# Performance work log

Measured on AMD Instinct MI355X. Metric: run time of the kernel, lower is better.

Reference implementation:

```python
import jax, jax.numpy as jnp
import numpy as np

T, N, E = 8, 10000, 200000
F_IN, H, OUT = 32, 128, 64
EPS = 1e-5


def setup_inputs() -> dict:
    key = jax.random.key(0)
    ks = jax.random.split(key, 28)
    inp = {}
    inp['x'] = jax.random.normal(ks[0], (T, N, F_IN), jnp.float32)
    inp['edge_index'] = jax.random.randint(ks[1], (2, E), 0, N, dtype=jnp.int32)
    # GCN layer weights (Glorot-ish scale)
    inp['w_gcn0'] = jax.random.normal(ks[2], (F_IN, H), jnp.float32) / np.float32(np.sqrt(F_IN))
    inp['b_gcn0'] = jnp.zeros((H,), jnp.float32)
    inp['w_gcn1'] = jax.random.normal(ks[3], (H, H), jnp.float32) / np.float32(np.sqrt(H))
    inp['b_gcn1'] = jnp.zeros((H,), jnp.float32)
    inp['w_gcn2'] = jax.random.normal(ks[4], (H, H), jnp.float32) / np.float32(np.sqrt(H))
    inp['b_gcn2'] = jnp.zeros((H,), jnp.float32)
    # BatchNorm (eval mode) params for the two inner norms
    for i, kb in zip(range(2), range(5, 9, 2)):
        inp[f'bn_g{i}'] = 1.0 + 0.1 * jax.random.normal(ks[kb], (H,), jnp.float32)
        inp[f'bn_b{i}'] = 0.1 * jax.random.normal(ks[kb + 1], (H,), jnp.float32)
        inp[f'bn_m{i}'] = 0.1 * jax.random.normal(ks[kb + 10], (H,), jnp.float32)
        inp[f'bn_v{i}'] = jax.random.uniform(ks[kb + 11], (H,), jnp.float32, 0.5, 1.5)
    # 3-layer LSTM params, torch gate order (i, f, g, o)
    s = np.float32(1.0 / np.sqrt(OUT))
    dims_in = [H, OUT, OUT]
    for l in range(3):
        k0, k1, k2, k3 = jax.random.split(ks[20 + l], 4)
        inp[f'w_ih_{l}'] = jax.random.uniform(k0, (4 * OUT, dims_in[l]), jnp.float32, -s, s)
        inp[f'w_hh_{l}'] = jax.random.uniform(k1, (4 * OUT, OUT), jnp.float32, -s, s)
        inp[f'b_ih_{l}'] = jax.random.uniform(k2, (4 * OUT,), jnp.float32, -s, s)
        inp[f'b_hh_{l}'] = jax.random.uniform(k3, (4 * OUT,), jnp.float32, -s, s)
    return inp


def reference(x, edge_index, w_gcn0, b_gcn0, w_gcn1, b_gcn1, w_gcn2, b_gcn2,
              bn_g0, bn_b0, bn_m0, bn_v0, bn_g1, bn_b1, bn_m1, bn_v1,
              w_ih_0, w_hh_0, b_ih_0, b_hh_0,
              w_ih_1, w_hh_1, b_ih_1, b_hh_1,
              w_ih_2, w_hh_2, b_ih_2, b_hh_2):
    src, dst = edge_index[0], edge_index[1]
    # symmetric GCN normalization with self-loops: deg = in-degree + 1
    deg = jax.ops.segment_sum(jnp.ones((E,), x.dtype), dst, num_segments=N) + 1.0
    dis = jax.lax.rsqrt(deg)
    coef = dis[src] * dis[dst]          # [E] edge norm
    self_w = dis * dis                   # [N] self-loop norm

    def gcn(h, W, b):
        hw = jnp.einsum('tnf,fo->tno', h, W)                      # [T,N,O]
        msg = hw[:, src, :] * coef[None, :, None]                  # [T,E,O]
        agg = jax.vmap(lambda m: jax.ops.segment_sum(m, dst, num_segments=N))(msg)
        return agg + hw * self_w[None, :, None] + b

    def bn(h, g, b_, m, v):  # eval-mode BatchNorm1d
        return (h - m) * (g * jax.lax.rsqrt(v + EPS)) + b_

    h = bn(jax.nn.relu(gcn(x, w_gcn0, b_gcn0)), bn_g0, bn_b0, bn_m0, bn_v0)
    h = bn(jax.nn.relu(gcn(h, w_gcn1, b_gcn1)), bn_g1, bn_b1, bn_m1, bn_v1)
    h = jax.nn.relu(gcn(h, w_gcn2, b_gcn2))                        # [T,N,H]

    def lstm_layer(xs, Wih, Whh, bih, bhh):
        Hd = Whh.shape[1]
        bias = bih + bhh
        def step(carry, xt):
            hp, cp = carry
            g = xt @ Wih.T + hp @ Whh.T + bias
            i, f, gg, o = jnp.split(g, 4, axis=-1)
            c = jax.nn.sigmoid(f) * cp + jax.nn.sigmoid(i) * jnp.tanh(gg)
            hn = jax.nn.sigmoid(o) * jnp.tanh(c)
            return (hn, c), hn
        z = jnp.zeros((xs.shape[1], Hd), xs.dtype)
        _, ys = jax.lax.scan(step, (z, z), xs)
        return ys  # [T,N,Hd]

    ys = lstm_layer(h, w_ih_0, w_hh_0, b_ih_0, b_hh_0)
    ys = lstm_layer(ys, w_ih_1, w_hh_1, b_ih_1, b_hh_1)
    ys = lstm_layer(ys, w_ih_2, w_hh_2, b_ih_2, b_hh_2)
    return ys[-1]  # [N, OUT] == x[:, -1, :] in the torch code
```

## Files before the change

### kernel.cpp

```cpp
#include <hip/hip_runtime.h>
#include <hip/hip_bf16.h>
#include <math.h>

#define NTHREADS 256
#define T_STEPS 8
#define F_INC 32
#define H_DIM 128
#define O_DIM 64

typedef unsigned short u16;
typedef __attribute__((ext_vector_type(8))) short short8_t;
typedef __attribute__((ext_vector_type(4))) float float4_t;
typedef __attribute__((ext_vector_type(2))) float float2_t;

__device__ __forceinline__ float bf2f(u16 u) {
    return __uint_as_float(((unsigned)u) << 16);
}
__device__ __forceinline__ u16 f2bf(float f) {
    __hip_bfloat16 h = __float2bfloat16(f);
    union { __hip_bfloat16 h; u16 s; } cv; cv.h = h; return cv.s;
}
__device__ __forceinline__ float2_t bfpair(unsigned u) {
    union { unsigned w[2]; float2_t f; } c;
    c.w[0] = u << 16;
    c.w[1] = u & 0xffff0000u;
    return c.f;
}
__device__ __forceinline__ void bf8_unpack(uint4 u, float* f) {
    f[0] = __uint_as_float(u.x << 16); f[1] = __uint_as_float(u.x & 0xffff0000u);
    f[2] = __uint_as_float(u.y << 16); f[3] = __uint_as_float(u.y & 0xffff0000u);
    f[4] = __uint_as_float(u.z << 16); f[5] = __uint_as_float(u.z & 0xffff0000u);
    f[6] = __uint_as_float(u.w << 16); f[7] = __uint_as_float(u.w & 0xffff0000u);
}
__device__ __forceinline__ float fsig(float x) {
    float xc = fminf(fmaxf(x, -30.f), 30.f);
    float e = __builtin_amdgcn_exp2f(xc * -1.4426950408889634f);
    return __builtin_amdgcn_rcpf(1.0f + e);
}
__device__ __forceinline__ float ftanh(float x) {
    float xc = fminf(fmaxf(x, -15.f), 15.f);
    float e = __builtin_amdgcn_exp2f(xc * -2.8853900817779268f);
    float r = __builtin_amdgcn_rcpf(1.0f + e);
    return fmaf(-2.0f * e, r, 1.0f);
}

__global__ void count_kernel(const int* __restrict__ ei, int* __restrict__ cnt, int E) {
    int e = blockIdx.x * NTHREADS + threadIdx.x;
    if (e < E) atomicAdd(&cnt[ei[E + e]], 1);
}

__global__ void scan_part1(const int* __restrict__ cnt, int* __restrict__ bsum, int n) {
    __shared__ int sd[NTHREADS];
    const int i = blockIdx.x * NTHREADS + threadIdx.x;
    sd[threadIdx.x] = (i < n) ? cnt[i] : 0;
    __syncthreads();
    for (int off = 128; off > 0; off >>= 1) {
        if (threadIdx.x < off) sd[threadIdx.x] += sd[threadIdx.x + off];
        __syncthreads();
    }
    if (threadIdx.x == 0) bsum[blockIdx.x] = sd[0];
}

__global__ void scan_part3(const int* __restrict__ cnt, const int* __restrict__ bsum,
                           int* __restrict__ rowptr, int* __restrict__ wp,
                           float* __restrict__ dis, float* __restrict__ selfw, int n) {
    __shared__ int sd[NTHREADS];
    __shared__ int sbase;
    const int tid = threadIdx.x;
    if (tid < 64) {
        int v0 = (tid < blockIdx.x) ? bsum[tid] : 0;
        #pragma unroll
        for (int off = 1; off < 64; off <<= 1) v0 += __shfl_xor(v0, off);
        if (tid == 0) sbase = v0;
    }
    const int i = blockIdx.x * NTHREADS + tid;
    const int v = (i < n) ? cnt[i] : 0;
    sd[tid] = v;
    __syncthreads();
    for (int off = 1; off < NTHREADS; off <<= 1) {
        const int tv = (tid >= off) ? sd[tid - off] : 0;
        __syncthreads();
        sd[tid] += tv;
        __syncthreads();
    }
    const int excl = sbase + sd[tid] - v;
    if (i < n) {
        rowptr[i] = excl; wp[i] = excl;
        if (i == n - 1) rowptr[n] = excl + v;
        const float d = 1.0f + (float)v;
        dis[i] = rsqrtf(d);
        selfw[i] = 1.0f / d;
    }
}

__global__ void fill_kernel(const int* __restrict__ ei, const float* __restrict__ dis,
                            int* __restrict__ wp, int2* __restrict__ epk, int E) {
    int e = blockIdx.x * NTHREADS + threadIdx.x;
    if (e < E) {
        int s = ei[e], d = ei[E + e];
        int p = atomicAdd(&wp[d], 1);
        epk[p] = make_int2(s, __float_as_int(dis[s] * dis[d]));
    }
}

__global__ void wprep_all_kernel(const float* g0, const float* g1, const float* g2,
                                 const float* i0, const float* i1, const float* i2,
                                 const float* h0, const float* h1, const float* h2,
                                 u16* o_g0, u16* o_g1, u16* o_g2,
                                 u16* o_i0, u16* o_i1, u16* o_i2,
                                 u16* o_h0, u16* o_h1, u16* o_h2) {
    const int i = blockIdx.x * NTHREADS + threadIdx.x;
    if (i < 4096)        { o_g0[i] = f2bf(g0[(i & 31) * 128 + (i >> 5)]); }
    else if (i < 20480)  { int j = i - 4096;   o_g1[j] = f2bf(g1[(j & 127) * 128 + (j >> 7)]); }
    else if (i < 36864)  { int j = i - 20480;  o_g2[j] = f2bf(g2[(j & 127) * 128 + (j >> 7)]); }
    else if (i < 69632)  { int j = i - 36864;  o_i0[j] = f2bf(i0[j]); }
    else if (i < 86016)  { int j = i - 69632;  o_i1[j] = f2bf(i1[j]); }
    else if (i < 102400) { int j = i - 86016;  o_i2[j] = f2bf(i2[j]); }
    else if (i < 118784) { int j = i - 102400; o_h0[j] = f2bf(h0[j]); }
    else if (i < 135168) { int j = i - 118784; o_h1[j] = f2bf(h1[j]); }
    else if (i < 151552) { int j = i - 135168; o_h2[j] = f2bf(h2[j]); }
}

__global__ __launch_bounds__(NTHREADS)
void gcn32_kernel(const float* __restrict__ x, const int* __restrict__ rowptr,
                  const int2* __restrict__ epk,
                  const float* __restrict__ selfw, const u16* __restrict__ Wt,
                  const float* __restrict__ bias,
                  const float* __restrict__ bng, const float* __restrict__ bnb,
                  const float* __restrict__ bnm, const float* __restrict__ bnv,
                  u16* __restrict__ out, int N) {
    constexpr int ASTR = 40;
    constexpr int ECAP = 1024;
    __shared__ __align__(16) u16 aT[2][16][ASTR];
    __shared__ int2 sM[ECAP];
    const int t0 = blockIdx.x * 2;
    const int n0 = blockIdx.y * 16;
    const int tid = threadIdx.x;
    const int wid = tid >> 6, lane = tid & 63;
    const int quad = lane >> 4, l16 = lane & 15;
    const float* xb0 = x + (long)t0 * N * 32;
    const float* xb1 = xb0 + (long)N * 32;

    const int eb0 = rowptr[n0];
    const int ecnt = min(rowptr[n0 + 16] - eb0, ECAP);
    for (int p = tid; p < ecnt; p += NTHREADS) sM[p] = epk[eb0 + p];
    __syncthreads();

    const int split = lane >> 3;
    const int c4 = (lane & 7) * 4;
    for (int i = 0; i < 4; ++i) {
        const int n = n0 + wid * 4 + i;
        const int l0 = rowptr[n] - eb0;
        const int l1 = rowptr[n + 1] - eb0;
        const int eL = min(l1, ecnt);
        const int start = l0 + split;
        float2_t a0[2] = {(float2_t){0.f, 0.f}, (float2_t){0.f, 0.f}};
        float2_t a1[2] = {(float2_t){0.f, 0.f}, (float2_t){0.f, 0.f}};
        #pragma unroll 2
        for (int e = start; e < eL; e += 8) {
            const int2 m = sM[e];
            const float w = __int_as_float(m.y);
            const float2_t w2 = {w, w};
            const long o = (long)m.x * 32 + c4;
            const float4 v0 = *(const float4*)(xb0 + o);
            const float4 v1 = *(const float4*)(xb1 + o);
            a0[0] = __builtin_elementwise_fma((float2_t){v0.x, v0.y}, w2, a0[0]);
            a0[1] = __builtin_elementwise_fma((float2_t){v0.z, v0.w}, w2, a0[1]);
            a1[0] = __builtin_elementwise_fma((float2_t){v1.x, v1.y}, w2, a1[0]);
            a1[1] = __builtin_elementwise_fma((float2_t){v1.z, v1.w}, w2, a1[1]);
        }
        const int kL = (eL > start) ? (eL - start + 7) >> 3 : 0;
        for (int e = start + kL * 8; e < l1; e += 8) {
            const int2 m = epk[eb0 + e];
            const float w = __int_as_float(m.y);
            const float2_t w2 = {w, w};
            const long o = (long)m.x * 32 + c4;
            const float4 v0 = *(const float4*)(xb0 + o);
            const float4 v1 = *(const float4*)(xb1 + o);
            a0[0] = __builtin_elementwise_fma((float2_t){v0.x, v0.y}, w2, a0[0]);
            a0[1] = __builtin_elementwise_fma((float2_t){v0.z, v0.w}, w2, a0[1]);
            a1[0] = __builtin_elementwise_fma((float2_t){v1.x, v1.y}, w2, a1[0]);
            a1[1] = __builtin_elementwise_fma((float2_t){v1.z, v1.w}, w2, a1[1]);
        }
        float r[8] = {a0[0][0], a0[0][1], a0[1][0], a0[1][1],
                      a1[0][0], a1[0][1], a1[1][0], a1[1][1]};
        #pragma unroll
        for (int j = 0; j < 8; ++j) {
            r[j] += __shfl_xor(r[j], 8);
            r[j] += __shfl_xor(r[j], 16);
            r[j] += __shfl_xor(r[j], 32);
        }
        if (split == 0) {
            const float sw = selfw[n];
            const float4 s0 = *(const float4*)(xb0 + (long)n * 32 + c4);
            const float4 s1 = *(const float4*)(xb1 + (long)n * 32 + c4);
            ushort4 o0, o1;
            o0.x = f2bf(fmaf(sw, s0.x, r[0])); o0.y = f2bf(fmaf(sw, s0.y, r[1]));
            o0.z = f2bf(fmaf(sw, s0.z, r[2])); o0.w = f2bf(fmaf(sw, s0.w, r[3]));
            o1.x = f2bf(fmaf(sw, s1.x, r[4])); o1.y = f2bf(fmaf(sw, s1.y, r[5]));
            o1.z = f2bf(fmaf(sw, s1.z, r[6])); o1.w = f2bf(fmaf(sw, s1.w, r[7]));
            *(ushort4*)(&aT[0][wid * 4 + i][c4]) = o0;
            *(ushort4*)(&aT[1][wid * 4 + i][c4]) = o1;
        }
    }
    __syncthreads();

    const short8_t fA0 = *(const short8_t*)(&aT[0][l16][quad * 8]);
    const short8_t fA1 = *(const short8_t*)(&aT[1][l16][quad * 8]);
    float4_t acc[2][2];
    short8_t fB[2];
    #pragma unroll
    for (int ct = 0; ct < 2; ++ct) {
        const int col = wid * 32 + ct * 16 + l16;
        fB[ct] = *(const short8_t*)(Wt + (long)col * 32 + quad * 8);
        acc[0][ct] = (float4_t){0.f, 0.f, 0.f, 0.f};
        acc[1][ct] = (float4_t){0.f, 0.f, 0.f, 0.f};
    }
    #pragma unroll
    for (int ct = 0; ct < 2; ++ct) {
        acc[0][ct] = __builtin_amdgcn_mfma_f32_16x16x32_bf16(fA0, fB[ct], acc[0][ct], 0, 0, 0);
        acc[1][ct] = __builtin_amdgcn_mfma_f32_16x16x32_bf16(fA1, fB[ct], acc[1][ct], 0, 0, 0);
    }

    #pragma unroll
    for (int ct = 0; ct < 2; ++ct) {
        const int c = wid * 32 + ct * 16 + l16;
        const float s = bng[c] * rsqrtf(bnv[c] + 1e-5f);
        const float a1 = bnb[c] - bnm[c] * s;
        const float a0 = bias[c];
        #pragma unroll
        for (int tt = 0; tt < 2; ++tt) {
            #pragma unroll
            for (int r = 0; r < 4; ++r) {
                const int node = quad * 4 + r;
                float v = fmaf(fmaxf(acc[tt][ct][r] + a0, 0.f), s, a1);
                out[((long)(t0 + tt) * N + n0 + node) * 128 + c] = f2bf(v);
            }
        }
    }
}

template<int EPI>
__global__ __launch_bounds__(NTHREADS)
void gcn128_kernel(const u16* __restrict__ h, const int* __restrict__ rowptr,
                   const int2* __restrict__ epk,
                   const float* __restrict__ selfw, const u16* __restrict__ Wt,
                   const float* __restrict__ bias,
                   const float* __restrict__ bng, const float* __restrict__ bnb,
                   const float* __restrict__ bnm, const float* __restrict__ bnv,
                   u16* __restrict__ out, int N) {
    constexpr int ASTR = 136;
    constexpr int ECAP = 1024;
    __shared__ __align__(16) u16 aT[16][ASTR];
    __shared__ int2 sM[ECAP];
    const int t = blockIdx.x;
    const int n0 = blockIdx.y * 16;
    const int tid = threadIdx.x;
    const int wid = tid >> 6, lane = tid & 63;
    const int quad = lane >> 4, l16 = lane & 15;
    const u16* hb = h + (long)t * N * 128;

    const int eb0 = rowptr[n0];
    const int ecnt = min(rowptr[n0 + 16] - eb0, ECAP);
    for (int p = tid; p < ecnt; p += NTHREADS) sM[p] = epk[eb0 + p];
    __syncthreads();

    const int split = lane >> 4;
    const int c8 = l16 * 8;
    for (int i = 0; i < 4; ++i) {
        const int n = n0 + wid * 4 + i;
        const int l0 = rowptr[n] - eb0;
        const int l1 = rowptr[n + 1] - eb0;
        const int eL = min(l1, ecnt);
        const int start = l0 + split;
        float2_t a2[4] = {(float2_t){0.f, 0.f}, (float2_t){0.f, 0.f},
                          (float2_t){0.f, 0.f}, (float2_t){0.f, 0.f}};
        #pragma unroll 4
        for (int e = start; e < eL; e += 4) {
            const int2 m = sM[e];
            const float w = __int_as_float(m.y);
            const float2_t w2 = {w, w};
            const uint4 v = *(const uint4*)(hb + (long)m.x * 128 + c8);
            a2[0] = __builtin_elementwise_fma(bfpair(v.x), w2, a2[0]);
            a2[1] = __builtin_elementwise_fma(bfpair(v.y), w2, a2[1]);
            a2[2] = __builtin_elementwise_fma(bfpair(v.z), w2, a2[2]);
            a2[3] = __builtin_elementwise_fma(bfpair(v.w), w2, a2[3]);
        }
        const int kL = (eL > start) ? (eL - start + 3) >> 2 : 0;
        for (int e = start + kL * 4; e < l1; e += 4) {
            const int2 m = epk[eb0 + e];
            const float w = __int_as_float(m.y);
            const float2_t w2 = {w, w};
            const uint4 v = *(const uint4*)(hb + (long)m.x * 128 + c8);
            a2[0] = __builtin_elementwise_fma(bfpair(v.x), w2, a2[0]);
            a2[1] = __builtin_elementwise_fma(bfpair(v.y), w2, a2[1]);
            a2[2] = __builtin_elementwise_fma(bfpair(v.z), w2, a2[2]);
            a2[3] = __builtin_elementwise_fma(bfpair(v.w), w2, a2[3]);
        }
        float a[8] = {a2[0][0], a2[0][1], a2[1][0], a2[1][1],
                      a2[2][0], a2[2][1], a2[3][0], a2[3][1]};
        #pragma unroll
        for (int j = 0; j < 8; ++j) {
            a[j] += __shfl_xor(a[j], 16);
            a[j] += __shfl_xor(a[j], 32);
        }
        if (split == 0) {
            const float sw = selfw[n];
            const uint4 sv = *(const uint4*)(hb + (long)n * 128 + c8);
            float f[8];
            bf8_unpack(sv, f);
            ushort4 o0, o1;
            o0.x = f2bf(fmaf(sw, f[0], a[0])); o0.y = f2bf(fmaf(sw, f[1], a[1]));
            o0.z = f2bf(fmaf(sw, f[2], a[2])); o0.w = f2bf(fmaf(sw, f[3], a[3]));
            o1.x = f2bf(fmaf(sw, f[4], a[4])); o1.y = f2bf(fmaf(sw, f[5], a[5]));
            o1.z = f2bf(fmaf(sw, f[6], a[6])); o1.w = f2bf(fmaf(sw, f[7], a[7]));
            *(ushort4*)(&aT[wid * 4 + i][c8]) = o0;
            *(ushort4*)(&aT[wid * 4 + i][c8 + 4]) = o1;
        }
    }
    __syncthreads();

    short8_t fA[4];
    #pragma unroll
    for (int ks = 0; ks < 4; ++ks)
        fA[ks] = *(const short8_t*)(&aT[l16][ks * 32 + quad * 8]);
    float4_t acc[2];
    #pragma unroll
    for (int ct = 0; ct < 2; ++ct) acc[ct] = (float4_t){0.f, 0.f, 0.f, 0.f};
    #pragma unroll
    for (int ct = 0; ct < 2; ++ct) {
        const int col = wid * 32 + ct * 16 + l16;
        #pragma unroll
        for (int ks = 0; ks < 4; ++ks) {
            const short8_t fB = *(const short8_t*)(Wt + (long)col * 128 + ks * 32 + quad * 8);
            acc[ct] = __builtin_amdgcn_mfma_f32_16x16x32_bf16(fA[ks], fB, acc[ct], 0, 0, 0);
        }
    }

    #pragma unroll
    for (int ct = 0; ct < 2; ++ct) {
        const int c = wid * 32 + ct * 16 + l16;
        const float a0 = bias[c];
        float s = 0.f, a1 = 0.f;
        if constexpr (EPI == 2) {
            s = bng[c] * rsqrtf(bnv[c] + 1e-5f);
            a1 = bnb[c] - bnm[c] * s;
        }
        #pragma unroll
        for (int r = 0; r < 4; ++r) {
            const int node = quad * 4 + r;
            float v = fmaxf(acc[ct][r] + a0, 0.f);
            if constexpr (EPI == 2) v = fmaf(v, s, a1);
            out[((long)t * N + n0 + node) * 128 + c] = f2bf(v);
        }
    }
}

template<int KIN, bool IN_SPLIT, bool LAST>
__global__ __launch_bounds__(NTHREADS, 2)
void lstm_layer_kernel(const u16* __restrict__ in_hi, const u16* __restrict__ in_lo,
                       const u16* __restrict__ wih, const u16* __restrict__ whh,
                       const float* __restrict__ bi, const float* __restrict__ bh,
                       u16* __restrict__ out_hi, u16* __restrict__ out_lo,
                       float* __restrict__ out_f, int N) {
    constexpr int NKS = KIN / 32;
    constexpr int HSTR = 76;
    const int tid = threadIdx.x;
    const int w = tid >> 6, lane = tid & 63;
    const int quad = lane >> 4, l16 = lane & 15;
    const int n0 = blockIdx.x * 16;
    const int u = w * 16 + l16;

    __shared__ __align__(16) u16 hT[2][16][HSTR];
    for (int p = tid; p < 2 * 16 * HSTR; p += NTHREADS) (&hT[0][0][0])[p] = 0;

    short8_t fI[4][NKS], fH[4][2];
    #pragma unroll
    for (int g = 0; g < 4; ++g) {
        #pragma unroll
        for (int ks = 0; ks < NKS; ++ks)
            fI[g][ks] = *(const short8_t*)(wih + (long)(g * 64 + u) * KIN + ks * 32 + quad * 8);
        #pragma unroll
        for (int ks = 0; ks < 2; ++ks)
            fH[g][ks] = *(const short8_t*)(whh + (long)(g * 64 + u) * 64 + ks * 32 + quad * 8);
    }
    float bias[4];
    #pragma unroll
    for (int g = 0; g < 4; ++g) bias[g] = bi[g * 64 + u] + bh[g * 64 + u];
    float cst[4] = {};
    __syncthreads();

    #pragma unroll 1
    for (int t = 0; t < T_STEPS; ++t) {
        short8_t ain[NKS], ainl[NKS];
        const long ibase = ((long)t * N + n0 + l16) * KIN + quad * 8;
        #pragma unroll
        for (int ks = 0; ks < NKS; ++ks) {
            ain[ks] = *(const short8_t*)(in_hi + ibase + ks * 32);
            if constexpr (IN_SPLIT) ainl[ks] = *(const short8_t*)(in_lo + ibase + ks * 32);
        }
        short8_t ah[2], al[2];
        #pragma unroll
        for (int ks = 0; ks < 2; ++ks) {
            ah[ks] = *(const short8_t*)(&hT[0][l16][ks * 32 + quad * 8]);
            al[ks] = *(const short8_t*)(&hT[1][l16][ks * 32 + quad * 8]);
        }
        __syncthreads();

        float4_t acc[4];
        #pragma unroll
        for (int g = 0; g < 4; ++g) acc[g] = (float4_t){bias[g], bias[g], bias[g], bias[g]};
        #pragma unroll
        for (int ks = 0; ks < NKS; ++ks)
            #pragma unroll
            for (int g = 0; g < 4; ++g) {
                acc[g] = __builtin_amdgcn_mfma_f32_16x16x32_bf16(ain[ks], fI[g][ks], acc[g], 0, 0, 0);
                if constexpr (IN_SPLIT)
                    acc[g] = __builtin_amdgcn_mfma_f32_16x16x32_bf16(ainl[ks], fI[g][ks], acc[g], 0, 0, 0);
            }
        #pragma unroll
        for (int ks = 0; ks < 2; ++ks)
            #pragma unroll
            for (int g = 0; g < 4; ++g) {
                acc[g] = __builtin_amdgcn_mfma_f32_16x16x32_bf16(ah[ks], fH[g][ks], acc[g], 0, 0, 0);
                acc[g] = __builtin_amdgcn_mfma_f32_16x16x32_bf16(al[ks], fH[g][ks], acc[g], 0, 0, 0);
            }

        #pragma unroll
        for (int r = 0; r < 4; ++r) {
            const float si = fsig(acc[0][r]);
            const float sf = fsig(acc[1][r]);
            const float gg = ftanh(acc[2][r]);
            const float so = fsig(acc[3][r]);
            const float c = sf * cst[r] + si * gg;
            cst[r] = c;
            const float h = so * ftanh(c);
            const int node = quad * 4 + r;
            const u16 hi = f2bf(h);
            const u16 lo = f2bf(h - bf2f(hi));
            hT[0][node][u] = hi;
            hT[1][node][u] = lo;
            if constexpr (LAST) {
                if (t == T_STEPS - 1) out_f[(long)(n0 + node) * 64 + u] = h;
            } else {
                const long o = ((long)t * N + n0 + node) * 64 + u;
                out_hi[o] = hi;
                out_lo[o] = lo;
            }
        }
        __syncthreads();
    }
}

extern "C" void kernel_launch(void* const* d_in, const int* in_sizes, int n_in,
                              void* d_out, int out_size, void* d_ws, size_t ws_size,
                              hipStream_t stream) {
    (void)n_in; (void)out_size; (void)ws_size;
    const float* x      = (const float*)d_in[0];
    const int*   ei     = (const int*)d_in[1];
    const float* w_gcn0 = (const float*)d_in[2];
    const float* b_gcn0 = (const float*)d_in[3];
    const float* w_gcn1 = (const float*)d_in[4];
    const float* b_gcn1 = (const float*)d_in[5];
    const float* w_gcn2 = (const float*)d_in[6];
    const float* b_gcn2 = (const float*)d_in[7];
    const float* bn_g0  = (const float*)d_in[8];
    const float* bn_b0  = (const float*)d_in[9];
    const float* bn_m0  = (const float*)d_in[10];
    const float* bn_v0  = (const float*)d_in[11];
    const float* bn_g1  = (const float*)d_in[12];
    const float* bn_b1  = (const float*)d_in[13];
    const float* bn_m1  = (const float*)d_in[14];
    const float* bn_v1  = (const float*)d_in[15];
    const float* w_ih_0 = (const float*)d_in[16];
    const float* w_hh_0 = (const float*)d_in[17];
    const float* b_ih_0 = (const float*)d_in[18];
    const float* b_hh_0 = (const float*)d_in[19];
    const float* w_ih_1 = (const float*)d_in[20];
    const float* w_hh_1 = (const float*)d_in[21];
    const float* b_ih_1 = (const float*)d_in[22];
    const float* b_hh_1 = (const float*)d_in[23];
    const float* w_ih_2 = (const float*)d_in[24];
    const float* w_hh_2 = (const float*)d_in[25];
    const float* b_ih_2 = (const float*)d_in[26];
    const float* b_hh_2 = (const float*)d_in[27];

    const int E = in_sizes[1] / 2;
    const int N = in_sizes[0] / (T_STEPS * F_INC);
    const long M = (long)N * T_STEPS;

    char* ws = (char*)d_ws;
    size_t off = 0;
    auto carve = [&](size_t bytes) -> void* {
        void* p = ws + off;
        off += (bytes + 255) & ~(size_t)255;
        return p;
    };
    float* dis     = (float*)carve((size_t)N * 4);
    float* selfw   = (float*)carve((size_t)N * 4);
    int*   cnt     = (int*)carve((size_t)N * 4);
    int*   rowptr  = (int*)carve((size_t)(N + 1) * 4);
    int*   wp      = (int*)carve((size_t)N * 4);
    int2*  epk     = (int2*)carve((size_t)E * 8);
    int*   bsum    = (int*)carve(64 * 4);
    u16*   hbuf    = (u16*)carve((size_t)M * H_DIM * 2);
    u16*   hbuf2   = (u16*)carve((size_t)M * H_DIM * 2);
    u16*   pA_hi   = (u16*)carve((size_t)M * O_DIM * 2);
    u16*   pA_lo   = (u16*)carve((size_t)M * O_DIM * 2);
    u16*   pB_hi   = (u16*)carve((size_t)M * O_DIM * 2);
    u16*   pB_lo   = (u16*)carve((size_t)M * O_DIM * 2);
    u16*   wt0     = (u16*)carve((size_t)128 * 32 * 2);
    u16*   wt1     = (u16*)carve((size_t)128 * 128 * 2);
    u16*   wt2     = (u16*)carve((size_t)128 * 128 * 2);
    u16*   wtih0   = (u16*)carve((size_t)256 * 128 * 2);
    u16*   wtih1   = (u16*)carve((size_t)256 * 64 * 2);
    u16*   wtih2   = (u16*)carve((size_t)256 * 64 * 2);
    u16*   whh0b   = (u16*)carve((size_t)256 * 64 * 2);
    u16*   whh1b   = (u16*)carve((size_t)256 * 64 * 2);
    u16*   whh2b   = (u16*)carve((size_t)256 * 64 * 2);

    const dim3 b256(NTHREADS);
    const int gN = (N + NTHREADS - 1) / NTHREADS;
    const int gE = (E + NTHREADS - 1) / NTHREADS;

    hipMemsetAsync(cnt, 0, (size_t)N * 4, stream);
    count_kernel<<<gE, b256, 0, stream>>>(ei, cnt, E);
    scan_part1<<<gN, b256, 0, stream>>>(cnt, bsum, N);
    scan_part3<<<gN, b256, 0, stream>>>(cnt, bsum, rowptr, wp, dis, selfw, N);
    fill_kernel<<<gE, b256, 0, stream>>>(ei, dis, wp, epk, E);

    wprep_all_kernel<<<(151552 + 255) / 256, b256, 0, stream>>>(
        w_gcn0, w_gcn1, w_gcn2, w_ih_0, w_ih_1, w_ih_2, w_hh_0, w_hh_1, w_hh_2,
        wt0, wt1, wt2, wtih0, wtih1, wtih2, whh0b, whh1b, whh2b);

    gcn32_kernel<<<dim3(T_STEPS / 2, N / 16), b256, 0, stream>>>(
        x, rowptr, epk, selfw, wt0, b_gcn0,
        bn_g0, bn_b0, bn_m0, bn_v0, hbuf, N);
    const dim3 gG(T_STEPS, N / 16);
    gcn128_kernel<2><<<gG, b256, 0, stream>>>(
        hbuf, rowptr, epk, selfw, wt1, b_gcn1,
        bn_g1, bn_b1, bn_m1, bn_v1, hbuf2, N);
    gcn128_kernel<1><<<gG, b256, 0, stream>>>(
        hbuf2, rowptr, epk, selfw, wt2, b_gcn2,
        nullptr, nullptr, nullptr, nullptr, hbuf, N);

    const int gL = N / 16;
    lstm_layer_kernel<128, false, false><<<gL, b256, 0, stream>>>(
        hbuf, nullptr, wtih0, whh0b, b_ih_0, b_hh_0, pA_hi, pA_lo, nullptr, N);
    lstm_layer_kernel<64, true, false><<<gL, b256, 0, stream>>>(
        pA_hi, pA_lo, wtih1, whh1b, b_ih_1, b_hh_1, pB_hi, pB_lo, nullptr, N);
    lstm_layer_kernel<64, true, true><<<gL, b256, 0, stream>>>(
        pB_hi, pB_lo, wtih2, whh2b, b_ih_2, b_hh_2, nullptr, nullptr, (float*)d_out, N);
}
```

Before: 356.6 us.

## Fuse LSTM layers 1-2, process two timesteps per GCN128 block, merge prep kernels

Runs LSTM layers 1 and 2 together in a single kernel, passing layer-1 hidden state to layer 2 through shared memory. This removes the intermediate hi/lo global buffers and one launch. The GCN128 kernel now handles two timesteps per block, so the CSR edge list is staged once and the weight fragments are reused across both timesteps. The degree-count kernel is merged with the weight-prep kernel to save another launch. In exchange, the fused kernels use more registers and shared memory, and the GCN128 grid has half as many blocks.

```diff
diff --git a/kernel.cpp b/kernel.cpp
--- a/kernel.cpp
+++ b/kernel.cpp
@@ -44,72 +44,20 @@
     return fmaf(-2.0f * e, r, 1.0f);
 }
 
-__global__ void count_kernel(const int* __restrict__ ei, int* __restrict__ cnt, int E) {
-    int e = blockIdx.x * NTHREADS + threadIdx.x;
-    if (e < E) atomicAdd(&cnt[ei[E + e]], 1);
-}
-
-__global__ void scan_part1(const int* __restrict__ cnt, int* __restrict__ bsum, int n) {
-    __shared__ int sd[NTHREADS];
-    const int i = blockIdx.x * NTHREADS + threadIdx.x;
-    sd[threadIdx.x] = (i < n) ? cnt[i] : 0;
-    __syncthreads();
-    for (int off = 128; off > 0; off >>= 1) {
-        if (threadIdx.x < off) sd[threadIdx.x] += sd[threadIdx.x + off];
-        __syncthreads();
-    }
-    if (threadIdx.x == 0) bsum[blockIdx.x] = sd[0];
-}
-
-__global__ void scan_part3(const int* __restrict__ cnt, const int* __restrict__ bsum,
-                           int* __restrict__ rowptr, int* __restrict__ wp,
-                           float* __restrict__ dis, float* __restrict__ selfw, int n) {
-    __shared__ int sd[NTHREADS];
-    __shared__ int sbase;
-    const int tid = threadIdx.x;
-    if (tid < 64) {
-        int v0 = (tid < blockIdx.x) ? bsum[tid] : 0;
-        #pragma unroll
-        for (int off = 1; off < 64; off <<= 1) v0 += __shfl_xor(v0, off);
-        if (tid == 0) sbase = v0;
-    }
-    const int i = blockIdx.x * NTHREADS + tid;
-    const int v = (i < n) ? cnt[i] : 0;
-    sd[tid] = v;
-    __syncthreads();
-    for (int off = 1; off < NTHREADS; off <<= 1) {
-        const int tv = (tid >= off) ? sd[tid - off] : 0;
-        __syncthreads();
-        sd[tid] += tv;
-        __syncthreads();
-    }
-    const int excl = sbase + sd[tid] - v;
-    if (i < n) {
-        rowptr[i] = excl; wp[i] = excl;
-        if (i == n - 1) rowptr[n] = excl + v;
-        const float d = 1.0f + (float)v;
-        dis[i] = rsqrtf(d);
-        selfw[i] = 1.0f / d;
-    }
-}
-
-__global__ void fill_kernel(const int* __restrict__ ei, const float* __restrict__ dis,
-                            int* __restrict__ wp, int2* __restrict__ epk, int E) {
-    int e = blockIdx.x * NTHREADS + threadIdx.x;
-    if (e < E) {
-        int s = ei[e], d = ei[E + e];
-        int p = atomicAdd(&wp[d], 1);
-        epk[p] = make_int2(s, __float_as_int(dis[s] * dis[d]));
-    }
-}
-
-__global__ void wprep_all_kernel(const float* g0, const float* g1, const float* g2,
-                                 const float* i0, const float* i1, const float* i2,
-                                 const float* h0, const float* h1, const float* h2,
-                                 u16* o_g0, u16* o_g1, u16* o_g2,
-                                 u16* o_i0, u16* o_i1, u16* o_i2,
-                                 u16* o_h0, u16* o_h1, u16* o_h2) {
-    const int i = blockIdx.x * NTHREADS + threadIdx.x;
+__global__ void count_wprep_kernel(const int* __restrict__ ei, int* __restrict__ cnt,
+                                   int E, int gE,
+                                   const float* g0, const float* g1, const float* g2,
+                                   const float* i0, const float* i1, const float* i2,
+                                   const float* h0, const float* h1, const float* h2,
+                                   u16* o_g0, u16* o_g1, u16* o_g2,
+                                   u16* o_i0, u16* o_i1, u16* o_i2,
+                                   u16* o_h0, u16* o_h1, u16* o_h2) {
+    if ((int)blockIdx.x < gE) {
+        int e = blockIdx.x * NTHREADS + threadIdx.x;
+        if (e < E) atomicAdd(&cnt[ei[E + e]], 1);
+        return;
+    }
+    const int i = (blockIdx.x - gE) * NTHREADS + threadIdx.x;
     if (i < 4096)        { o_g0[i] = f2bf(g0[(i & 31) * 128 + (i >> 5)]); }
     else if (i < 20480)  { int j = i - 4096;   o_g1[j] = f2bf(g1[(j & 127) * 128 + (j >> 7)]); }
     else if (i < 36864)  { int j = i - 20480;  o_g2[j] = f2bf(g2[(j & 127) * 128 + (j >> 7)]); }
@@ -119,6 +67,60 @@
     else if (i < 118784) { int j = i - 102400; o_h0[j] = f2bf(h0[j]); }
     else if (i < 135168) { int j = i - 118784; o_h1[j] = f2bf(h1[j]); }
     else if (i < 151552) { int j = i - 135168; o_h2[j] = f2bf(h2[j]); }
+}
+
+__global__ void scan_part1(const int* __restrict__ cnt, int* __restrict__ bsum, int n) {
+    __shared__ int sd[NTHREADS];
+    const int i = blockIdx.x * NTHREADS + threadIdx.x;
+    sd[threadIdx.x] = (i < n) ? cnt[i] : 0;
+    __syncthreads();
+    for (int off = 128; off > 0; off >>= 1) {
+        if (threadIdx.x < off) sd[threadIdx.x] += sd[threadIdx.x + off];
+        __syncthreads();
+    }
+    if (threadIdx.x == 0) bsum[blockIdx.x] = sd[0];
+}
+
+__global__ void scan_part3(const int* __restrict__ cnt, const int* __restrict__ bsum,
+                           int* __restrict__ rowptr, int* __restrict__ wp,
+                           float* __restrict__ dis, float* __restrict__ selfw, int n) {
+    __shared__ int sd[NTHREADS];
+    __shared__ int sbase;
+    const int tid = threadIdx.x;
+    if (tid < 64) {
+        int v0 = (tid < blockIdx.x) ? bsum[tid] : 0;
+        #pragma unroll
+        for (int off = 1; off < 64; off <<= 1) v0 += __shfl_xor(v0, off);
+        if (tid == 0) sbase = v0;
+    }
+    const int i = blockIdx.x * NTHREADS + tid;
+    const int v = (i < n) ? cnt[i] : 0;
+    sd[tid] = v;
+    __syncthreads();
+    for (int off = 1; off < NTHREADS; off <<= 1) {
+        const int tv = (tid >= off) ? sd[tid - off] : 0;
+        __syncthreads();
+        sd[tid] += tv;
+        __syncthreads();
+    }
+    const int excl = sbase + sd[tid] - v;
+    if (i < n) {
+        rowptr[i] = excl; wp[i] = excl;
+        if (i == n - 1) rowptr[n] = excl + v;
+        const float d = 1.0f + (float)v;
+        dis[i] = rsqrtf(d);
+        selfw[i] = 1.0f / d;
+    }
+}
+
+__global__ void fill_kernel(const int* __restrict__ ei, const float* __restrict__ dis,
+                            int* __restrict__ wp, int2* __restrict__ epk, int E) {
+    int e = blockIdx.x * NTHREADS + threadIdx.x;
+    if (e < E) {
+        int s = ei[e], d = ei[E + e];
+        int p = atomicAdd(&wp[d], 1);
+        epk[p] = make_int2(s, __float_as_int(dis[s] * dis[d]));
+    }
 }
 
 __global__ __launch_bounds__(NTHREADS)
@@ -251,14 +253,15 @@
                    u16* __restrict__ out, int N) {
     constexpr int ASTR = 136;
     constexpr int ECAP = 1024;
-    __shared__ __align__(16) u16 aT[16][ASTR];
+    __shared__ __align__(16) u16 aT[2][16][ASTR];
     __shared__ int2 sM[ECAP];
-    const int t = blockIdx.x;
+    const int t0 = blockIdx.x * 2;
     const int n0 = blockIdx.y * 16;
     const int tid = threadIdx.x;
     const int wid = tid >> 6, lane = tid & 63;
     const int quad = lane >> 4, l16 = lane & 15;
-    const u16* hb = h + (long)t * N * 128;
+    const u16* hb0 = h + (long)t0 * N * 128;
+    const u16* hb1 = hb0 + (long)N * 128;
 
     const int eb0 = rowptr[n0];
     const int ecnt = min(rowptr[n0 + 16] - eb0, ECAP);
@@ -273,67 +276,96 @@
         const int l1 = rowptr[n + 1] - eb0;
         const int eL = min(l1, ecnt);
         const int start = l0 + split;
-        float2_t a2[4] = {(float2_t){0.f, 0.f}, (float2_t){0.f, 0.f},
+        float2_t aA[4] = {(float2_t){0.f, 0.f}, (float2_t){0.f, 0.f},
+                          (float2_t){0.f, 0.f}, (float2_t){0.f, 0.f}};
+        float2_t aB[4] = {(float2_t){0.f, 0.f}, (float2_t){0.f, 0.f},
                           (float2_t){0.f, 0.f}, (float2_t){0.f, 0.f}};
         #pragma unroll 4
         for (int e = start; e < eL; e += 4) {
             const int2 m = sM[e];
             const float w = __int_as_float(m.y);
             const float2_t w2 = {w, w};
-            const uint4 v = *(const uint4*)(hb + (long)m.x * 128 + c8);
-            a2[0] = __builtin_elementwise_fma(bfpair(v.x), w2, a2[0]);
-            a2[1] = __builtin_elementwise_fma(bfpair(v.y), w2, a2[1]);
-            a2[2] = __builtin_elementwise_fma(bfpair(v.z), w2, a2[2]);
-            a2[3] = __builtin_elementwise_fma(bfpair(v.w), w2, a2[3]);
+            const long o = (long)m.x * 128 + c8;
+            const uint4 v0 = *(const uint4*)(hb0 + o);
+            const uint4 v1 = *(const uint4*)(hb1 + o);
+            aA[0] = __builtin_elementwise_fma(bfpair(v0.x), w2, aA[0]);
+            aA[1] = __builtin_elementwise_fma(bfpair(v0.y), w2, aA[1]);
+            aA[2] = __builtin_elementwise_fma(bfpair(v0.z), w2, aA[2]);
+            aA[3] = __builtin_elementwise_fma(bfpair(v0.w), w2, aA[3]);
+            aB[0] = __builtin_elementwise_fma(bfpair(v1.x), w2, aB[0]);
+            aB[1] = __builtin_elementwise_fma(bfpair(v1.y), w2, aB[1]);
+            aB[2] = __builtin_elementwise_fma(bfpair(v1.z), w2, aB[2]);
+            aB[3] = __builtin_elementwise_fma(bfpair(v1.w), w2, aB[3]);
         }
         const int kL = (eL > start) ? (eL - start + 3) >> 2 : 0;
         for (int e = start + kL * 4; e < l1; e += 4) {
             const int2 m = epk[eb0 + e];
             const float w = __int_as_float(m.y);
             const float2_t w2 = {w, w};
-            const uint4 v = *(const uint4*)(hb + (long)m.x * 128 + c8);
-            a2[0] = __builtin_elementwise_fma(bfpair(v.x), w2, a2[0]);
-            a2[1] = __builtin_elementwise_fma(bfpair(v.y), w2, a2[1]);
-            a2[2] = __builtin_elementwise_fma(bfpair(v.z), w2, a2[2]);
-            a2[3] = __builtin_elementwise_fma(bfpair(v.w), w2, a2[3]);
-        }
-        float a[8] = {a2[0][0], a2[0][1], a2[1][0], a2[1][1],
-                      a2[2][0], a2[2][1], a2[3][0], a2[3][1]};
-        #pragma unroll
-        for (int j = 0; j < 8; ++j) {
+            const long o = (long)m.x * 128 + c8;
+            const uint4 v0 = *(const uint4*)(hb0 + o);
+            const uint4 v1 = *(const uint4*)(hb1 + o);
+            aA[0] = __builtin_elementwise_fma(bfpair(v0.x), w2, aA[0]);
+            aA[1] = __builtin_elementwise_fma(bfpair(v0.y), w2, aA[1]);
+            aA[2] = __builtin_elementwise_fma(bfpair(v0.z), w2, aA[2]);
+            aA[3] = __builtin_elementwise_fma(bfpair(v0.w), w2, aA[3]);
+            aB[0] = __builtin_elementwise_fma(bfpair(v1.x), w2, aB[0]);
+            aB[1] = __builtin_elementwise_fma(bfpair(v1.y), w2, aB[1]);
+            aB[2] = __builtin_elementwise_fma(bfpair(v1.z), w2, aB[2]);
+            aB[3] = __builtin_elementwise_fma(bfpair(v1.w), w2, aB[3]);
+        }
+        float a[16] = {aA[0][0], aA[0][1], aA[1][0], aA[1][1],
+                       aA[2][0], aA[2][1], aA[3][0], aA[3][1],
+                       aB[0][0], aB[0][1], aB[1][0], aB[1][1],
+                       aB[2][0], aB[2][1], aB[3][0], aB[3][1]};
+        #pragma unroll
+        for (int j = 0; j < 16; ++j) {
             a[j] += __shfl_xor(a[j], 16);
             a[j] += __shfl_xor(a[j], 32);
         }
         if (split == 0) {
             const float sw = selfw[n];
-            const uint4 sv = *(const uint4*)(hb + (long)n * 128 + c8);
-            float f[8];
-            bf8_unpack(sv, f);
-            ushort4 o0, o1;
-            o0.x = f2bf(fmaf(sw, f[0], a[0])); o0.y = f2bf(fmaf(sw, f[1], a[1]));
-            o0.z = f2bf(fmaf(sw, f[2], a[2])); o0.w = f2bf(fmaf(sw, f[3], a[3]));
-            o1.x = f2bf(fmaf(sw, f[4], a[4])); o1.y = f2bf(fmaf(sw, f[5], a[5]));
-            o1.z = f2bf(fmaf(sw, f[6], a[6])); o1.w = f2bf(fmaf(sw, f[7], a[7]));
-            *(ushort4*)(&aT[wid * 4 + i][c8]) = o0;
-            *(ushort4*)(&aT[wid * 4 + i][c8 + 4]) = o1;
-        }
-    }
-    __syncthreads();
-
-    short8_t fA[4];
-    #pragma unroll
-    for (int ks = 0; ks < 4; ++ks)
-        fA[ks] = *(const short8_t*)(&aT[l16][ks * 32 + quad * 8]);
-    float4_t acc[2];
-    #pragma unroll
-    for (int ct = 0; ct < 2; ++ct) acc[ct] = (float4_t){0.f, 0.f, 0.f, 0.f};
+            const uint4 s0 = *(const uint4*)(hb0 + (long)n * 128 + c8);
+            const uint4 s1 = *(const uint4*)(hb1 + (long)n * 128 + c8);
+            float f0[8], f1[8];
+            bf8_unpack(s0, f0);
+            bf8_unpack(s1, f1);
+            ushort4 oA0, oA1, oB0, oB1;
+            oA0.x = f2bf(fmaf(sw, f0[0], a[0]));  oA0.y = f2bf(fmaf(sw, f0[1], a[1]));
+            oA0.z = f2bf(fmaf(sw, f0[2], a[2]));  oA0.w = f2bf(fmaf(sw, f0[3], a[3]));
+            oA1.x = f2bf(fmaf(sw, f0[4], a[4]));  oA1.y = f2bf(fmaf(sw, f0[5], a[5]));
+            oA1.z = f2bf(fmaf(sw, f0[6], a[6]));  oA1.w = f2bf(fmaf(sw, f0[7], a[7]));
+            oB0.x = f2bf(fmaf(sw, f1[0], a[8]));  oB0.y = f2bf(fmaf(sw, f1[1], a[9]));
+            oB0.z = f2bf(fmaf(sw, f1[2], a[10])); oB0.w = f2bf(fmaf(sw, f1[3], a[11]));
+            oB1.x = f2bf(fmaf(sw, f1[4], a[12])); oB1.y = f2bf(fmaf(sw, f1[5], a[13]));
+            oB1.z = f2bf(fmaf(sw, f1[6], a[14])); oB1.w = f2bf(fmaf(sw, f1[7], a[15]));
+            *(ushort4*)(&aT[0][wid * 4 + i][c8]) = oA0;
+            *(ushort4*)(&aT[0][wid * 4 + i][c8 + 4]) = oA1;
+            *(ushort4*)(&aT[1][wid * 4 + i][c8]) = oB0;
+            *(ushort4*)(&aT[1][wid * 4 + i][c8 + 4]) = oB1;
+        }
+    }
+    __syncthreads();
+
+    short8_t fA0[4], fA1[4];
+    #pragma unroll
+    for (int ks = 0; ks < 4; ++ks) {
+        fA0[ks] = *(const short8_t*)(&aT[0][l16][ks * 32 + quad * 8]);
+        fA1[ks] = *(const short8_t*)(&aT[1][l16][ks * 32 + quad * 8]);
+    }
+    float4_t acc[2][2];
+    #pragma unroll
+    for (int tt = 0; tt < 2; ++tt)
+        #pragma unroll
+        for (int ct = 0; ct < 2; ++ct) acc[tt][ct] = (float4_t){0.f, 0.f, 0.f, 0.f};
     #pragma unroll
     for (int ct = 0; ct < 2; ++ct) {
         const int col = wid * 32 + ct * 16 + l16;
         #pragma unroll
         for (int ks = 0; ks < 4; ++ks) {
             const short8_t fB = *(const short8_t*)(Wt + (long)col * 128 + ks * 32 + quad * 8);
-            acc[ct] = __builtin_amdgcn_mfma_f32_16x16x32_bf16(fA[ks], fB, acc[ct], 0, 0, 0);
+            acc[0][ct] = __builtin_amdgcn_mfma_f32_16x16x32_bf16(fA0[ks], fB, acc[0][ct], 0, 0, 0);
+            acc[1][ct] = __builtin_amdgcn_mfma_f32_16x16x32_bf16(fA1[ks], fB, acc[1][ct], 0, 0, 0);
         }
     }
 
@@ -347,23 +379,23 @@
             a1 = bnb[c] - bnm[c] * s;
         }
         #pragma unroll
-        for (int r = 0; r < 4; ++r) {
-            const int node = quad * 4 + r;
-            float v = fmaxf(acc[ct][r] + a0, 0.f);
-            if constexpr (EPI == 2) v = fmaf(v, s, a1);
-            out[((long)t * N + n0 + node) * 128 + c] = f2bf(v);
-        }
-    }
-}
-
-template<int KIN, bool IN_SPLIT, bool LAST>
+        for (int tt = 0; tt < 2; ++tt) {
+            #pragma unroll
+            for (int r = 0; r < 4; ++r) {
+                const int node = quad * 4 + r;
+                float v = fmaxf(acc[tt][ct][r] + a0, 0.f);
+                if constexpr (EPI == 2) v = fmaf(v, s, a1);
+                out[((long)(t0 + tt) * N + n0 + node) * 128 + c] = f2bf(v);
+            }
+        }
+    }
+}
+
 __global__ __launch_bounds__(NTHREADS, 2)
-void lstm_layer_kernel(const u16* __restrict__ in_hi, const u16* __restrict__ in_lo,
-                       const u16* __restrict__ wih, const u16* __restrict__ whh,
-                       const float* __restrict__ bi, const float* __restrict__ bh,
-                       u16* __restrict__ out_hi, u16* __restrict__ out_lo,
-                       float* __restrict__ out_f, int N) {
-    constexpr int NKS = KIN / 32;
+void lstm0_kernel(const u16* __restrict__ in_h, const u16* __restrict__ wih,
+                  const u16* __restrict__ whh,
+                  const float* __restrict__ bi, const float* __restrict__ bh,
+                  u16* __restrict__ out_hi, u16* __restrict__ out_lo, int N) {
     constexpr int HSTR = 76;
     const int tid = threadIdx.x;
     const int w = tid >> 6, lane = tid & 63;
@@ -374,12 +406,12 @@
     __shared__ __align__(16) u16 hT[2][16][HSTR];
     for (int p = tid; p < 2 * 16 * HSTR; p += NTHREADS) (&hT[0][0][0])[p] = 0;
 
-    short8_t fI[4][NKS], fH[4][2];
+    short8_t fI[4][4], fH[4][2];
     #pragma unroll
     for (int g = 0; g < 4; ++g) {
         #pragma unroll
-        for (int ks = 0; ks < NKS; ++ks)
-            fI[g][ks] = *(const short8_t*)(wih + (long)(g * 64 + u) * KIN + ks * 32 + quad * 8);
+        for (int ks = 0; ks < 4; ++ks)
+            fI[g][ks] = *(const short8_t*)(wih + (long)(g * 64 + u) * 128 + ks * 32 + quad * 8);
         #pragma unroll
         for (int ks = 0; ks < 2; ++ks)
             fH[g][ks] = *(const short8_t*)(whh + (long)(g * 64 + u) * 64 + ks * 32 + quad * 8);
@@ -392,13 +424,11 @@
 
     #pragma unroll 1
     for (int t = 0; t < T_STEPS; ++t) {
-        short8_t ain[NKS], ainl[NKS];
-        const long ibase = ((long)t * N + n0 + l16) * KIN + quad * 8;
-        #pragma unroll
-        for (int ks = 0; ks < NKS; ++ks) {
-            ain[ks] = *(const short8_t*)(in_hi + ibase + ks * 32);
-            if constexpr (IN_SPLIT) ainl[ks] = *(const short8_t*)(in_lo + ibase + ks * 32);
-        }
+        short8_t ain[4];
+        const long ibase = ((long)t * N + n0 + l16) * 128 + quad * 8;
+        #pragma unroll
+        for (int ks = 0; ks < 4; ++ks)
+            ain[ks] = *(const short8_t*)(in_h + ibase + ks * 32);
         short8_t ah[2], al[2];
         #pragma unroll
         for (int ks = 0; ks < 2; ++ks) {
@@ -411,13 +441,10 @@
         #pragma unroll
         for (int g = 0; g < 4; ++g) acc[g] = (float4_t){bias[g], bias[g], bias[g], bias[g]};
         #pragma unroll
-        for (int ks = 0; ks < NKS; ++ks)
+        for (int ks = 0; ks < 4; ++ks)
             #pragma unroll
-            for (int g = 0; g < 4; ++g) {
+            for (int g = 0; g < 4; ++g)
                 acc[g] = __builtin_amdgcn_mfma_f32_16x16x32_bf16(ain[ks], fI[g][ks], acc[g], 0, 0, 0);
-                if constexpr (IN_SPLIT)
-                    acc[g] = __builtin_amdgcn_mfma_f32_16x16x32_bf16(ainl[ks], fI[g][ks], acc[g], 0, 0, 0);
-            }
         #pragma unroll
         for (int ks = 0; ks < 2; ++ks)
             #pragma unroll
@@ -440,12 +467,126 @@
             const u16 lo = f2bf(h - bf2f(hi));
             hT[0][node][u] = hi;
             hT[1][node][u] = lo;
-            if constexpr (LAST) {
-                if (t == T_STEPS - 1) out_f[(long)(n0 + node) * 64 + u] = h;
+            const long o = ((long)t * N + n0 + node) * 64 + u;
+            out_hi[o] = hi;
+            out_lo[o] = lo;
+        }
+        __syncthreads();
+    }
+}
+
+__global__ __launch_bounds__(NTHREADS)
+void lstm12_kernel(const u16* __restrict__ in_hi, const u16* __restrict__ in_lo,
+                   const u16* __restrict__ wih1, const u16* __restrict__ whh1,
+                   const u16* __restrict__ wih2, const u16* __restrict__ whh2,
+                   const float* __restrict__ bi1, const float* __restrict__ bh1,
+                   const float* __restrict__ bi2, const float* __restrict__ bh2,
+                   float* __restrict__ out_f, int N) {
+    constexpr int HSTR = 76;
+    const int tid = threadIdx.x;
+    const int w = tid >> 6, lane = tid & 63;
+    const int quad = lane >> 4, l16 = lane & 15;
+    const int n0 = blockIdx.x * 16;
+    const int u = w * 16 + l16;
+
+    __shared__ __align__(16) u16 hT[2][2][16][HSTR];
+    for (int p = tid; p < 2 * 2 * 16 * HSTR; p += NTHREADS) (&hT[0][0][0][0])[p] = 0;
+
+    short8_t fI1[4][2], fH1[4][2], fI2[4][2], fH2[4][2];
+    #pragma unroll
+    for (int g = 0; g < 4; ++g)
+        #pragma unroll
+        for (int ks = 0; ks < 2; ++ks) {
+            fI1[g][ks] = *(const short8_t*)(wih1 + (long)(g * 64 + u) * 64 + ks * 32 + quad * 8);
+            fH1[g][ks] = *(const short8_t*)(whh1 + (long)(g * 64 + u) * 64 + ks * 32 + quad * 8);
+            fI2[g][ks] = *(const short8_t*)(wih2 + (long)(g * 64 + u) * 64 + ks * 32 + quad * 8);
+            fH2[g][ks] = *(const short8_t*)(whh2 + (long)(g * 64 + u) * 64 + ks * 32 + quad * 8);
+        }
+    float b1[4], b2[4];
+    #pragma unroll
+    for (int g = 0; g < 4; ++g) {
+        b1[g] = bi1[g * 64 + u] + bh1[g * 64 + u];
+        b2[g] = bi2[g * 64 + u] + bh2[g * 64 + u];
+    }
+    float c1[4] = {}, c2[4] = {};
+    __syncthreads();
+
+    #pragma unroll 1
+    for (int t = 0; t < T_STEPS; ++t) {
+        short8_t ainh[2], ainl[2], r1h[2], r1l[2], r2h[2], r2l[2];
+        const long ibase = ((long)t * N + n0 + l16) * 64 + quad * 8;
+        #pragma unroll
+        for (int ks = 0; ks < 2; ++ks) {
+            ainh[ks] = *(const short8_t*)(in_hi + ibase + ks * 32);
+            ainl[ks] = *(const short8_t*)(in_lo + ibase + ks * 32);
+            r1h[ks] = *(const short8_t*)(&hT[0][0][l16][ks * 32 + quad * 8]);
+            r1l[ks] = *(const short8_t*)(&hT[0][1][l16][ks * 32 + quad * 8]);
+            r2h[ks] = *(const short8_t*)(&hT[1][0][l16][ks * 32 + quad * 8]);
+            r2l[ks] = *(const short8_t*)(&hT[1][1][l16][ks * 32 + quad * 8]);
+        }
+        __syncthreads();
+
+        float4_t acc[4];
+        #pragma unroll
+        for (int g = 0; g < 4; ++g) acc[g] = (float4_t){b1[g], b1[g], b1[g], b1[g]};
+        #pragma unroll
+        for (int ks = 0; ks < 2; ++ks)
+            #pragma unroll
+            for (int g = 0; g < 4; ++g) {
+                acc[g] = __builtin_amdgcn_mfma_f32_16x16x32_bf16(ainh[ks], fI1[g][ks], acc[g], 0, 0, 0);
+                acc[g] = __builtin_amdgcn_mfma_f32_16x16x32_bf16(ainl[ks], fI1[g][ks], acc[g], 0, 0, 0);
+                acc[g] = __builtin_amdgcn_mfma_f32_16x16x32_bf16(r1h[ks], fH1[g][ks], acc[g], 0, 0, 0);
+                acc[g] = __builtin_amdgcn_mfma_f32_16x16x32_bf16(r1l[ks], fH1[g][ks], acc[g], 0, 0, 0);
+            }
+        #pragma unroll
+        for (int r = 0; r < 4; ++r) {
+            const float si = fsig(acc[0][r]);
+            const float sf = fsig(acc[1][r]);
+            const float gg = ftanh(acc[2][r]);
+            const float so = fsig(acc[3][r]);
+            const float c = sf * c1[r] + si * gg;
+            c1[r] = c;
+            const float h = so * ftanh(c);
+            const int node = quad * 4 + r;
+            const u16 hi = f2bf(h);
+            hT[0][0][node][u] = hi;
+            hT[0][1][node][u] = f2bf(h - bf2f(hi));
+        }
+        __syncthreads();
+
+        short8_t i2h[2], i2l[2];
+        #pragma unroll
+        for (int ks = 0; ks < 2; ++ks) {
+            i2h[ks] = *(const short8_t*)(&hT[0][0][l16][ks * 32 + quad * 8]);
+            i2l[ks] = *(const short8_t*)(&hT[0][1][l16][ks * 32 + quad * 8]);
+        }
+        #pragma unroll
+        for (int g = 0; g < 4; ++g) acc[g] = (float4_t){b2[g], b2[g], b2[g], b2[g]};
+        #pragma unroll
+        for (int ks = 0; ks < 2; ++ks)
+            #pragma unroll
+            for (int g = 0; g < 4; ++g) {
+                acc[g] = __builtin_amdgcn_mfma_f32_16x16x32_bf16(i2h[ks], fI2[g][ks], acc[g], 0, 0, 0);
+                acc[g] = __builtin_amdgcn_mfma_f32_16x16x32_bf16(i2l[ks], fI2[g][ks], acc[g], 0, 0, 0);
+                acc[g] = __builtin_amdgcn_mfma_f32_16x16x32_bf16(r2h[ks], fH2[g][ks], acc[g], 0, 0, 0);
+                acc[g] = __builtin_amdgcn_mfma_f32_16x16x32_bf16(r2l[ks], fH2[g][ks], acc[g], 0, 0, 0);
+            }
+        #pragma unroll
+        for (int r = 0; r < 4; ++r) {
+            const float si = fsig(acc[0][r]);
+            const float sf = fsig(acc[1][r]);
+            const float gg = ftanh(acc[2][r]);
+            const float so = fsig(acc[3][r]);
+            const float c = sf * c2[r] + si * gg;
+            c2[r] = c;
+            const float h = so * ftanh(c);
+            const int node = quad * 4 + r;
+            if (t == T_STEPS - 1) {
+                out_f[(long)(n0 + node) * 64 + u] = h;
             } else {
-                const long o = ((long)t * N + n0 + node) * 64 + u;
-                out_hi[o] = hi;
-                out_lo[o] = lo;
+                const u16 hi = f2bf(h);
+                hT[1][0][node][u] = hi;
+                hT[1][1][node][u] = f2bf(h - bf2f(hi));
             }
         }
         __syncthreads();
@@ -507,8 +648,6 @@
     u16*   hbuf2   = (u16*)carve((size_t)M * H_DIM * 2);
     u16*   pA_hi   = (u16*)carve((size_t)M * O_DIM * 2);
     u16*   pA_lo   = (u16*)carve((size_t)M * O_DIM * 2);
-    u16*   pB_hi   = (u16*)carve((size_t)M * O_DIM * 2);
-    u16*   pB_lo   = (u16*)carve((size_t)M * O_DIM * 2);
     u16*   wt0     = (u16*)carve((size_t)128 * 32 * 2);
     u16*   wt1     = (u16*)carve((size_t)128 * 128 * 2);
     u16*   wt2     = (u16*)carve((size_t)128 * 128 * 2);
@@ -524,19 +663,18 @@
     const int gE = (E + NTHREADS - 1) / NTHREADS;
 
     hipMemsetAsync(cnt, 0, (size_t)N * 4, stream);
-    count_kernel<<<gE, b256, 0, stream>>>(ei, cnt, E);
+    count_wprep_kernel<<<gE + (151552 + 255) / 256, b256, 0, stream>>>(
+        ei, cnt, E, gE,
+        w_gcn0, w_gcn1, w_gcn2, w_ih_0, w_ih_1, w_ih_2, w_hh_0, w_hh_1, w_hh_2,
+        wt0, wt1, wt2, wtih0, wtih1, wtih2, whh0b, whh1b, whh2b);
     scan_part1<<<gN, b256, 0, stream>>>(cnt, bsum, N);
     scan_part3<<<gN, b256, 0, stream>>>(cnt, bsum, rowptr, wp, dis, selfw, N);
     fill_kernel<<<gE, b256, 0, stream>>>(ei, dis, wp, epk, E);
 
-    wprep_all_kernel<<<(151552 + 255) / 256, b256, 0, stream>>>(
-        w_gcn0, w_gcn1, w_gcn2, w_ih_0, w_ih_1, w_ih_2, w_hh_0, w_hh_1, w_hh_2,
-        wt0, wt1, wt2, wtih0, wtih1, wtih2, whh0b, whh1b, whh2b);
-
-    gcn32_kernel<<<dim3(T_STEPS / 2, N / 16), b256, 0, stream>>>(
+    const dim3 gG(T_STEPS / 2, N / 16);
+    gcn32_kernel<<<gG, b256, 0, stream>>>(
         x, rowptr, epk, selfw, wt0, b_gcn0,
         bn_g0, bn_b0, bn_m0, bn_v0, hbuf, N);
-    const dim3 gG(T_STEPS, N / 16);
     gcn128_kernel<2><<<gG, b256, 0, stream>>>(
         hbuf, rowptr, epk, selfw, wt1, b_gcn1,
         bn_g1, bn_b1, bn_m1, bn_v1, hbuf2, N);
@@ -545,10 +683,9 @@
         nullptr, nullptr, nullptr, nullptr, hbuf, N);
 
     const int gL = N / 16;
-    lstm_layer_kernel<128, false, false><<<gL, b256, 0, stream>>>(
-        hbuf, nullptr, wtih0, whh0b, b_ih_0, b_hh_0, pA_hi, pA_lo, nullptr, N);
-    lstm_layer_kernel<64, true, false><<<gL, b256, 0, stream>>>(
-        pA_hi, pA_lo, wtih1, whh1b, b_ih_1, b_hh_1, pB_hi, pB_lo, nullptr, N);
-    lstm_layer_kernel<64, true, true><<<gL, b256, 0, stream>>>(
-        pB_hi, pB_lo, wtih2, whh2b, b_ih_2, b_hh_2, nullptr, nullptr, (float*)d_out, N);
-}
+    lstm0_kernel<<<gL, b256, 0, stream>>>(
+        hbuf, wtih0, whh0b, b_ih_0, b_hh_0, pA_hi, pA_lo, N);
+    lstm12_kernel<<<gL, b256, 0, stream>>>(
+        pA_hi, pA_lo, wtih1, whh1b, wtih2, whh2b,
+        b_ih_1, b_hh_1, b_ih_2, b_hh_2, (float*)d_out, N);
+}
```

New measurement: 363.8 us. 1.02x slower.
